# Kernel tuning notes

Hardware: AMD Instinct MI355X
Metric: run time of the kernel (lower is better)

Reference implementation:

```python
import jax, jax.numpy as jnp
import numpy as np

N, E, F, H, G = 50000, 800000, 64, 64, 100

def setup_inputs() -> dict:
    key = jax.random.key(0)
    ks = jax.random.split(key, 12)
    x = jax.random.normal(ks[0], (N, F), dtype=jnp.float32)
    edge_index = jax.random.randint(ks[1], (2, E), 0, N, dtype=jnp.int64)
    batch = jnp.sort(jax.random.randint(ks[2], (N,), 0, G, dtype=jnp.int64))
    s1 = 1.0 / np.sqrt(F); s2 = 1.0 / np.sqrt(H)
    W1 = jax.random.normal(ks[3], (2, F, H), dtype=jnp.float32) * s1
    b1 = jnp.zeros((H,), dtype=jnp.float32)
    W2 = jax.random.normal(ks[4], (2, H, H), dtype=jnp.float32) * s2
    b2 = jnp.zeros((H,), dtype=jnp.float32)
    gamma = jnp.ones((H,), dtype=jnp.float32)
    beta = jnp.zeros((H,), dtype=jnp.float32)
    linW = jax.random.normal(ks[5], (H, 1), dtype=jnp.float32) * s2
    linb = jnp.zeros((1,), dtype=jnp.float32)
    return {"x": x, "edge_index": edge_index, "batch": batch, "W1": W1, "b1": b1,
            "W2": W2, "b2": b2, "gamma": gamma, "beta": beta, "linW": linW, "linb": linb}

def _edge_norm(row, col, n):
    # get_laplacian(sym) + lambda_max=2: Lhat off-diag weight = -d_i^{-1/2} d_j^{-1/2}, diag = 0
    deg = jax.ops.segment_sum(jnp.ones(row.shape[0], jnp.float32), row, num_segments=n)
    dis = jnp.where(deg > 0, deg ** -0.5, 0.0)
    return -dis[row] * dis[col]

def _cheb(x, row, col, w, W, b):
    # K=2: out = T0(Lhat)x @ W0 + T1(Lhat)x @ W1 + b, T1 = Lhat x via scatter-add
    Tx1 = jax.ops.segment_sum(w[:, None] * x[row], col, num_segments=x.shape[0])
    return x @ W[0] + Tx1 @ W[1] + b

def reference(x, edge_index, batch, W1, b1, W2, b2, gamma, beta, linW, linb):
    row, col = edge_index[0], edge_index[1]
    n = x.shape[0]
    w = _edge_norm(row, col, n)
    h = _cheb(x, row, col, w, W1, b1)
    # BatchNorm1d (training-mode batch stats, eps=1e-5)
    mu = jnp.mean(h, axis=0)
    var = jnp.var(h, axis=0)
    h = (h - mu) * jax.lax.rsqrt(var + 1e-5) * gamma + beta
    # LeakyReLU (default slope 0.01)
    h = jnp.where(h >= 0, h, 0.01 * h)
    h = _cheb(h, row, col, w, W2, b2)
    # global_mean_pool over graph ids
    sums = jax.ops.segment_sum(h, batch, num_segments=G)
    cnts = jax.ops.segment_sum(jnp.ones(n, jnp.float32), batch, num_segments=G)
    pooled = sums / jnp.maximum(cnts, 1.0)[:, None]
    # dropout: identity (eval)
    return pooled @ linW + linb
```

## Files before the change

### kernel.cpp

```cpp
#include <hip/hip_runtime.h>

#define HDIM 64
#define BH 64
#define HNODES 25600
#define HBINS 12800
#define SBINS 12544


__device__ __forceinline__ int lbound(const int* __restrict__ b, int n, int v) {
    int lo = 0, hi = n;
    while (lo < hi) { int m = (lo + hi) >> 1; if (b[m] < v) lo = m + 1; else hi = m; }
    return lo;
}


__global__ __launch_bounds__(256) void k_histP(const int* __restrict__ row,
                                               const int* __restrict__ col,
                                               unsigned short* __restrict__ cntP,
                                               unsigned short* __restrict__ degP,
                                               int E, int N, int slice) {
    __shared__ unsigned hbin[HBINS];
    int blk   = blockIdx.x;
    int phase = blockIdx.y & 1;
    int isRow = blockIdx.y >> 1;
    const int* keys = isRow ? row : col;
    unsigned short* outP = isRow ? degP : cntP;
    int lo = phase * HNODES;
    int spanN = min(HNODES, N - lo);
    int binsU = (spanN + 1) >> 1;
    for (int i = threadIdx.x; i < binsU; i += 256) hbin[i] = 0;
    __syncthreads();
    int e0 = blk * slice, e1 = min(e0 + slice, E);
    for (int e = e0 + threadIdx.x; e < e1; e += 256) {
        int c = keys[e] - lo;
        if ((unsigned)c < (unsigned)spanN)
            atomicAdd(&hbin[c >> 1], 1u << ((c & 1) << 4));
    }
    __syncthreads();
    unsigned* outU = (unsigned*)(outP + (size_t)blk * N + lo);
    for (int i = threadIdx.x; i < binsU; i += 256) outU[i] = hbin[i];
}

__global__ void k_prefA(unsigned short* __restrict__ cntP,
                        const unsigned short* __restrict__ degP,
                        int* __restrict__ cnt, float* __restrict__ dis, int N) {
    int i = blockIdx.x * blockDim.x + threadIdx.x;
    if (i >= N) return;
    int run = 0;
    #pragma unroll 8
    for (int b = 0; b < BH; ++b) {
        int v = cntP[(size_t)b * N + i];
        cntP[(size_t)b * N + i] = (unsigned short)run;
        run += v;
    }
    cnt[i] = run;
    int d = 0;
    #pragma unroll 8
    for (int b = 0; b < BH; ++b) d += degP[(size_t)b * N + i];
    dis[i] = d > 0 ? rsqrtf((float)d) : 0.0f;
}

__global__ __launch_bounds__(1024) void k_scan1(const int* __restrict__ cnt,
                                                int* __restrict__ start,
                                                int* __restrict__ bsum, int n) {
    __shared__ int sh[1024];
    int i = blockIdx.x * 1024 + threadIdx.x;
    int v = (i < n) ? cnt[i] : 0;
    sh[threadIdx.x] = v;
    __syncthreads();
    for (int off = 1; off < 1024; off <<= 1) {
        int t = 0;
        if (threadIdx.x >= off) t = sh[threadIdx.x - off];
        __syncthreads();
        sh[threadIdx.x] += t;
        __syncthreads();
    }
    if (i < n) start[i] = sh[threadIdx.x] - v;
    if (threadIdx.x == 1023) bsum[blockIdx.x] = sh[1023];
}

__global__ void k_scan2(int* __restrict__ bsum, int nb) {
    int lane = threadIdx.x;
    if (lane >= 64) return;
    int v = (lane < nb) ? bsum[lane] : 0;
    int incl = v;
    #pragma unroll
    for (int off = 1; off < 64; off <<= 1) {
        int u = __shfl_up(incl, off, 64);
        if (lane >= off) incl += u;
    }
    if (lane < nb) bsum[lane] = incl - v;
}

__global__ void k_scan3(int* __restrict__ start, const int* __restrict__ bsum, int n) {
    int i = blockIdx.x * blockDim.x + threadIdx.x;
    if (i < n) start[i] += bsum[i >> 10];
}

__global__ __launch_bounds__(256) void k_sortfill(const int* __restrict__ row,
                                                  const int* __restrict__ col,
                                                  const unsigned short* __restrict__ cntP,
                                                  const int* __restrict__ start,
                                                  int* __restrict__ er,
                                                  int E, int N, int slice) {
    __shared__ int cur[SBINS];
    int blk = blockIdx.x;
    int lo = blockIdx.y * SBINS;
    int span = min(SBINS, N - lo);
    for (int i = threadIdx.x; i < span; i += 256)
        cur[i] = start[lo + i] + (int)cntP[(size_t)blk * N + lo + i];
    __syncthreads();
    int e0 = blk * slice, e1 = min(e0 + slice, E);
    for (int e = e0 + threadIdx.x; e < e1; e += 256) {
        int c = col[e] - lo;
        int rv = row[e];
        if ((unsigned)c < (unsigned)span) {
            int pos = atomicAdd(&cur[c], 1);
            er[pos] = rv;
        }
    }
}


__global__ __launch_bounds__(256) void k_gather1(const int* __restrict__ er,
                                                 const int* __restrict__ start,
                                                 const int* __restrict__ cnt,
                                                 const float* __restrict__ dis,
                                                 const float* __restrict__ x,
                                                 float* __restrict__ Tx, int n) {
    int i = blockIdx.x * 4 + (threadIdx.x >> 6);
    if (i >= n) return;
    int lane = threadIdx.x & 63;
    int q = lane >> 4;
    int s4 = (lane & 15) * 4;
    int s = start[i], nd = cnt[i];
    float di = dis[i];
    float4 acc = make_float4(0.f, 0.f, 0.f, 0.f);
    int k = q;
    for (; k + 4 < nd; k += 8) {
        int r0 = er[s + k], r1 = er[s + k + 4];
        float w0 = -dis[r0] * di, w1 = -dis[r1] * di;
        float4 v0 = *reinterpret_cast<const float4*>(&x[(size_t)r0 * HDIM + s4]);
        float4 v1 = *reinterpret_cast<const float4*>(&x[(size_t)r1 * HDIM + s4]);
        acc.x = fmaf(w0, v0.x, acc.x); acc.y = fmaf(w0, v0.y, acc.y);
        acc.z = fmaf(w0, v0.z, acc.z); acc.w = fmaf(w0, v0.w, acc.w);
        acc.x = fmaf(w1, v1.x, acc.x); acc.y = fmaf(w1, v1.y, acc.y);
        acc.z = fmaf(w1, v1.z, acc.z); acc.w = fmaf(w1, v1.w, acc.w);
    }
    if (k < nd) {
        int r0 = er[s + k];
        float w0 = -dis[r0] * di;
        float4 v0 = *reinterpret_cast<const float4*>(&x[(size_t)r0 * HDIM + s4]);
        acc.x = fmaf(w0, v0.x, acc.x); acc.y = fmaf(w0, v0.y, acc.y);
        acc.z = fmaf(w0, v0.z, acc.z); acc.w = fmaf(w0, v0.w, acc.w);
    }
    #pragma unroll
    for (int off = 16; off <= 32; off <<= 1) {
        acc.x += __shfl_xor(acc.x, off, 64);
        acc.y += __shfl_xor(acc.y, off, 64);
        acc.z += __shfl_xor(acc.z, off, 64);
        acc.w += __shfl_xor(acc.w, off, 64);
    }
    if (q == 0) *reinterpret_cast<float4*>(&Tx[(size_t)i * HDIM + s4]) = acc;
}

__global__ __launch_bounds__(256) void k_gemm1(const float* __restrict__ x,
                                               float* __restrict__ TxH,
                                               const float* __restrict__ W1,
                                               const float* __restrict__ b1,
                                               float* __restrict__ stats, int n) {
    __shared__ float Ws[2 * HDIM * HDIM];
    __shared__ float xs[4][HDIM];
    __shared__ float ts[4][HDIM];
    int tid = threadIdx.x;
    for (int idx = tid; idx < 2 * HDIM * HDIM; idx += 256) Ws[idx] = W1[idx];

    int rr = tid >> 6;
    int j  = tid & 63;
    float bj = b1[j];
    const float* w0 = Ws;
    const float* w1 = Ws + HDIM * HDIM;
    float sacc = 0.f, ssacc = 0.f;

    for (int base = blockIdx.x * 4; base < n; base += gridDim.x * 4) {
        int r = base + rr;
        __syncthreads();
        if (r < n) {
            xs[rr][j] = x[(size_t)r * HDIM + j];
            ts[rr][j] = TxH[(size_t)r * HDIM + j];
        }
        __syncthreads();
        if (r < n) {
            float acc = bj;
            #pragma unroll 8
            for (int k = 0; k < HDIM; ++k) {
                acc = fmaf(xs[rr][k], w0[k * HDIM + j], acc);
                acc = fmaf(ts[rr][k], w1[k * HDIM + j], acc);
            }
            TxH[(size_t)r * HDIM + j] = acc;
            sacc += acc;
            ssacc = fmaf(acc, acc, ssacc);
        }
    }
    __syncthreads();
    xs[rr][j] = sacc;
    ts[rr][j] = ssacc;
    __syncthreads();
    if (rr == 0) {
        float s  = xs[0][j] + xs[1][j] + xs[2][j] + xs[3][j];
        float ss = ts[0][j] + ts[1][j] + ts[2][j] + ts[3][j];
        atomicAdd(&stats[j], s);
        atomicAdd(&stats[64 + j], ss);
    }
}

__global__ void k_prep(const float* __restrict__ stats,
                       const float* __restrict__ gamma, const float* __restrict__ beta,
                       const float* __restrict__ W2, const float* __restrict__ b2,
                       const float* __restrict__ linW, const float* __restrict__ linb,
                       float* __restrict__ scale, float* __restrict__ shift,
                       float* __restrict__ u0, float* __restrict__ u1,
                       float* __restrict__ c0, int n) {
    int k = threadIdx.x;
    if (k >= HDIM) return;
    float inv_n = 1.0f / (float)n;
    float mu  = stats[k] * inv_n;
    float var = stats[64 + k] * inv_n - mu * mu;
    float rs  = rsqrtf(var + 1e-5f);
    float sc  = rs * gamma[k];
    scale[k] = sc;
    shift[k] = beta[k] - mu * sc;
    float a0 = 0.f, a1 = 0.f;
    #pragma unroll 8
    for (int j = 0; j < HDIM; ++j) {
        float lw = linW[j];
        a0 = fmaf(W2[k * HDIM + j], lw, a0);
        a1 = fmaf(W2[HDIM * HDIM + k * HDIM + j], lw, a1);
    }
    u0[k] = a0;
    u1[k] = a1;
    if (k == 0) {
        float c = linb[0];
        for (int j = 0; j < HDIM; ++j) c = fmaf(b2[j], linW[j], c);
        c0[0] = c;
    }
}

__global__ __launch_bounds__(256) void k_node(const float* __restrict__ h,
                                              const float* __restrict__ scale,
                                              const float* __restrict__ shift,
                                              const float* __restrict__ u0,
                                              const float* __restrict__ u1,
                                              float* __restrict__ a, float* __restrict__ t,
                                              int n) {
    int i = blockIdx.x * 4 + (threadIdx.x >> 6);
    if (i >= n) return;
    int j = threadIdx.x & 63;
    float v = fmaf(h[(size_t)i * HDIM + j], scale[j], shift[j]);
    v = v >= 0.f ? v : 0.01f * v;
    float p0 = v * u0[j];
    float p1 = v * u1[j];
    #pragma unroll
    for (int off = 32; off > 0; off >>= 1) {
        p0 += __shfl_xor(p0, off, 64);
        p1 += __shfl_xor(p1, off, 64);
    }
    if (j == 0) { a[i] = p0; t[i] = p1; }
}

__global__ void k_gather2(const int* __restrict__ er, const int* __restrict__ start,
                          const int* __restrict__ cnt, const float* __restrict__ dis,
                          const float* __restrict__ t, const float* __restrict__ a,
                          float* __restrict__ s2, int n) {
    int i = blockIdx.x * blockDim.x + threadIdx.x;
    if (i >= n) return;
    int s = start[i], nd = cnt[i];
    float di = dis[i];
    float acc = a[i];
    int k = 0;
    for (; k + 1 < nd; k += 2) {
        int r0 = er[s + k], r1 = er[s + k + 1];
        float v0 = -dis[r0] * di * t[r0];
        float v1 = -dis[r1] * di * t[r1];
        acc += v0 + v1;
    }
    if (k < nd) {
        int r0 = er[s + k];
        acc = fmaf(-dis[r0] * di, t[r0], acc);
    }
    s2[i] = acc;
}

__global__ __launch_bounds__(256) void k_pool2(const float* __restrict__ s2,
                                               const int* __restrict__ batch,
                                               const float* __restrict__ c0,
                                               const float* __restrict__ linb,
                                               float* __restrict__ out, int n) {
    int g = blockIdx.x;
    int lo = lbound(batch, n, g);
    int hi = lbound(batch, n, g + 1);
    float s = 0.f;
    for (int i = lo + threadIdx.x; i < hi; i += 256) s += s2[i];
    __shared__ float red[256];
    red[threadIdx.x] = s;
    __syncthreads();
    for (int off = 128; off > 0; off >>= 1) {
        if (threadIdx.x < off) red[threadIdx.x] += red[threadIdx.x + off];
        __syncthreads();
    }
    if (threadIdx.x == 0) {
        int cntg = hi - lo;
        out[g] = cntg > 0 ? red[0] / (float)cntg + c0[0] : linb[0];
    }
}


extern "C" void kernel_launch(void* const* d_in, const int* in_sizes, int n_in,
                              void* d_out, int out_size, void* d_ws, size_t ws_size,
                              hipStream_t stream) {
    const float* x     = (const float*)d_in[0];
    const int*   eidx  = (const int*)d_in[1];
    const int*   batch = (const int*)d_in[2];
    const float* W1    = (const float*)d_in[3];
    const float* b1    = (const float*)d_in[4];
    const float* W2    = (const float*)d_in[5];
    const float* b2    = (const float*)d_in[6];
    const float* gamma = (const float*)d_in[7];
    const float* beta  = (const float*)d_in[8];
    const float* linW  = (const float*)d_in[9];
    const float* linb  = (const float*)d_in[10];
    float* out = (float*)d_out;

    const int N = in_sizes[0] / HDIM;
    const int E = in_sizes[1] / 2;
    const int G = out_size;
    const int NB = (N + 1023) / 1024;
    const int slice = (E + BH - 1) / BH;

    const int* row = eidx;
    const int* col = eidx + E;

    char* wsb = (char*)d_ws;
    float* TxH  = (float*)wsb;               wsb += (size_t)N * HDIM * 4;
    unsigned short* cntP = (unsigned short*)TxH;
    unsigned short* degP = cntP + (size_t)BH * N;
    int*   cnt   = (int*)wsb;                wsb += (size_t)N * 4;
    int*   start = (int*)wsb;                wsb += (size_t)N * 4;
    int*   bsum  = (int*)wsb;                wsb += (size_t)NB * 4 + 64;
    int*   er    = (int*)wsb;                wsb += (size_t)E * 4;
    float* dis   = (float*)wsb;              wsb += (size_t)N * 4;
    float* a     = (float*)wsb;              wsb += (size_t)N * 4;
    float* t     = (float*)wsb;              wsb += (size_t)N * 4;
    float* s2    = (float*)wsb;              wsb += (size_t)N * 4;
    float* stats = (float*)wsb;              wsb += 128 * 4;
    float* scale = (float*)wsb;              wsb += HDIM * 4;
    float* shift = (float*)wsb;              wsb += HDIM * 4;
    float* u0    = (float*)wsb;              wsb += HDIM * 4;
    float* u1    = (float*)wsb;              wsb += HDIM * 4;
    float* c0    = (float*)wsb;              wsb += 64;

    hipMemsetAsync(stats, 0, 128 * 4, stream);

    k_histP<<<dim3(BH, 4), 256, 0, stream>>>(row, col, cntP, degP, E, N, slice);
    k_prefA<<<(N + 255) / 256, 256, 0, stream>>>(cntP, degP, cnt, dis, N);
    k_scan1<<<NB, 1024, 0, stream>>>(cnt, start, bsum, N);
    k_scan2<<<1, 64, 0, stream>>>(bsum, NB);
    k_scan3<<<(N + 255) / 256, 256, 0, stream>>>(start, bsum, N);
    k_sortfill<<<dim3(BH, 4), 256, 0, stream>>>(row, col, cntP, start, er, E, N, slice);
    k_gather1<<<(N + 3) / 4, 256, 0, stream>>>(er, start, cnt, dis, x, TxH, N);
    k_gemm1<<<1024, 256, 0, stream>>>(x, TxH, W1, b1, stats, N);
    k_prep<<<1, 64, 0, stream>>>(stats, gamma, beta, W2, b2, linW, linb,
                                 scale, shift, u0, u1, c0, N);
    k_node<<<(N + 3) / 4, 256, 0, stream>>>(TxH, scale, shift, u0, u1, a, t, N);
    k_gather2<<<(N + 255) / 256, 256, 0, stream>>>(er, start, cnt, dis, t, a, s2, N);
    k_pool2<<<G, 256, 0, stream>>>(s2, batch, c0, linb, out, N);
}
```

Baseline: 209.3 us.

## Keep GEMM weights in registers, tile 32 rows per block, and use a wave-shuffle scan

Result: faster. 190.7 us (-8.9%).

```diff
diff --git a/kernel.cpp b/kernel.cpp
--- a/kernel.cpp
+++ b/kernel.cpp
@@ -5,6 +5,7 @@
 #define HNODES 25600
 #define HBINS 12800
 #define SBINS 12544
+#define GR 32
 
 
 __device__ __forceinline__ int lbound(const int* __restrict__ b, int n, int v) {
@@ -63,20 +64,32 @@
 __global__ __launch_bounds__(1024) void k_scan1(const int* __restrict__ cnt,
                                                 int* __restrict__ start,
                                                 int* __restrict__ bsum, int n) {
-    __shared__ int sh[1024];
+    __shared__ int wsum[16];
     int i = blockIdx.x * 1024 + threadIdx.x;
+    int lane = threadIdx.x & 63, w = threadIdx.x >> 6;
     int v = (i < n) ? cnt[i] : 0;
-    sh[threadIdx.x] = v;
-    __syncthreads();
-    for (int off = 1; off < 1024; off <<= 1) {
-        int t = 0;
-        if (threadIdx.x >= off) t = sh[threadIdx.x - off];
-        __syncthreads();
-        sh[threadIdx.x] += t;
-        __syncthreads();
-    }
-    if (i < n) start[i] = sh[threadIdx.x] - v;
-    if (threadIdx.x == 1023) bsum[blockIdx.x] = sh[1023];
+    int incl = v;
+    #pragma unroll
+    for (int off = 1; off < 64; off <<= 1) {
+        int u = __shfl_up(incl, off, 64);
+        if (lane >= off) incl += u;
+    }
+    if (lane == 63) wsum[w] = incl;
+    __syncthreads();
+    if (w == 0) {
+        int s = (lane < 16) ? wsum[lane] : 0;
+        int si = s;
+        #pragma unroll
+        for (int off = 1; off < 16; off <<= 1) {
+            int u = __shfl_up(si, off, 64);
+            if (lane >= off) si += u;
+        }
+        if (lane < 16) wsum[lane] = si - s;
+    }
+    __syncthreads();
+    int excl = incl - v + wsum[w];
+    if (i < n) start[i] = excl;
+    if (threadIdx.x == 1023) bsum[blockIdx.x] = excl + v;
 }
 
 __global__ void k_scan2(int* __restrict__ bsum, int nb) {
@@ -169,44 +182,68 @@
                                                const float* __restrict__ W1,
                                                const float* __restrict__ b1,
                                                float* __restrict__ stats, int n) {
-    __shared__ float Ws[2 * HDIM * HDIM];
-    __shared__ float xs[4][HDIM];
-    __shared__ float ts[4][HDIM];
+    __shared__ float xs[GR][HDIM];
+    __shared__ float ts[GR][HDIM];
     int tid = threadIdx.x;
-    for (int idx = tid; idx < 2 * HDIM * HDIM; idx += 256) Ws[idx] = W1[idx];
-
-    int rr = tid >> 6;
-    int j  = tid & 63;
+    int j = tid & 63, w = tid >> 6;
+
+    float4 w0r[16], w1r[16];
+    #pragma unroll
+    for (int k4 = 0; k4 < 16; ++k4) {
+        w0r[k4].x = W1[(k4 * 4 + 0) * HDIM + j];
+        w0r[k4].y = W1[(k4 * 4 + 1) * HDIM + j];
+        w0r[k4].z = W1[(k4 * 4 + 2) * HDIM + j];
+        w0r[k4].w = W1[(k4 * 4 + 3) * HDIM + j];
+        w1r[k4].x = W1[4096 + (k4 * 4 + 0) * HDIM + j];
+        w1r[k4].y = W1[4096 + (k4 * 4 + 1) * HDIM + j];
+        w1r[k4].z = W1[4096 + (k4 * 4 + 2) * HDIM + j];
+        w1r[k4].w = W1[4096 + (k4 * 4 + 3) * HDIM + j];
+    }
     float bj = b1[j];
-    const float* w0 = Ws;
-    const float* w1 = Ws + HDIM * HDIM;
     float sacc = 0.f, ssacc = 0.f;
 
-    for (int base = blockIdx.x * 4; base < n; base += gridDim.x * 4) {
-        int r = base + rr;
+    for (int base = blockIdx.x * GR; base < n; base += gridDim.x * GR) {
         __syncthreads();
-        if (r < n) {
-            xs[rr][j] = x[(size_t)r * HDIM + j];
-            ts[rr][j] = TxH[(size_t)r * HDIM + j];
+        for (int v = tid; v < GR * HDIM / 4; v += 256) {
+            int r = base + (v >> 4);
+            if (r < n) {
+                int c = (v & 15) * 4;
+                ((float4*)xs)[v] = *(const float4*)&x[(size_t)r * HDIM + c];
+                ((float4*)ts)[v] = *(const float4*)&TxH[(size_t)r * HDIM + c];
+            }
         }
         __syncthreads();
-        if (r < n) {
-            float acc = bj;
-            #pragma unroll 8
-            for (int k = 0; k < HDIM; ++k) {
-                acc = fmaf(xs[rr][k], w0[k * HDIM + j], acc);
-                acc = fmaf(ts[rr][k], w1[k * HDIM + j], acc);
+        #pragma unroll
+        for (int m = 0; m < 8; ++m) {
+            int lr = w * 8 + m;
+            int r = base + lr;
+            if (r < n) {
+                const float4* xr = (const float4*)xs[lr];
+                const float4* tr = (const float4*)ts[lr];
+                float acc = bj;
+                #pragma unroll
+                for (int k4 = 0; k4 < 16; ++k4) {
+                    float4 xv = xr[k4], tv = tr[k4];
+                    acc = fmaf(xv.x, w0r[k4].x, acc);
+                    acc = fmaf(xv.y, w0r[k4].y, acc);
+                    acc = fmaf(xv.z, w0r[k4].z, acc);
+                    acc = fmaf(xv.w, w0r[k4].w, acc);
+                    acc = fmaf(tv.x, w1r[k4].x, acc);
+                    acc = fmaf(tv.y, w1r[k4].y, acc);
+                    acc = fmaf(tv.z, w1r[k4].z, acc);
+                    acc = fmaf(tv.w, w1r[k4].w, acc);
+                }
+                TxH[(size_t)r * HDIM + j] = acc;
+                sacc += acc;
+                ssacc = fmaf(acc, acc, ssacc);
             }
-            TxH[(size_t)r * HDIM + j] = acc;
-            sacc += acc;
-            ssacc = fmaf(acc, acc, ssacc);
         }
     }
     __syncthreads();
-    xs[rr][j] = sacc;
-    ts[rr][j] = ssacc;
-    __syncthreads();
-    if (rr == 0) {
+    xs[w][j] = sacc;
+    ts[w][j] = ssacc;
+    __syncthreads();
+    if (w == 0) {
         float s  = xs[0][j] + xs[1][j] + xs[2][j] + xs[3][j];
         float ss = ts[0][j] + ts[1][j] + ts[2][j] + ts[3][j];
         atomicAdd(&stats[j], s);
@@ -368,7 +405,7 @@
     k_scan3<<<(N + 255) / 256, 256, 0, stream>>>(start, bsum, N);
     k_sortfill<<<dim3(BH, 4), 256, 0, stream>>>(row, col, cntP, start, er, E, N, slice);
     k_gather1<<<(N + 3) / 4, 256, 0, stream>>>(er, start, cnt, dis, x, TxH, N);
-    k_gemm1<<<1024, 256, 0, stream>>>(x, TxH, W1, b1, stats, N);
+    k_gemm1<<<512, 256, 0, stream>>>(x, TxH, W1, b1, stats, N);
     k_prep<<<1, 64, 0, stream>>>(stats, gamma, beta, W2, b2, linW, linb,
                                  scale, shift, u0, u1, c0, N);
     k_node<<<(N + 3) / 4, 256, 0, stream>>>(TxH, scale, shift, u0, u1, a, t, N);
```
